# Performance work log

Measured on AMD Instinct MI355X. Metric: run time of the kernel, lower is better.

## Reference

```python
import jax, jax.numpy as jnp
import numpy as np

B, T, D = 32, 2048, 512
BATCH_SIZE = 32  # config.batch_size: number of MVN draws


def setup_inputs() -> dict:
    key = jax.random.key(0)
    k1, k2 = jax.random.split(key)
    x = jax.random.normal(k1, (B, T, D), dtype=jnp.float32)
    z = jax.random.normal(k2, (BATCH_SIZE, D), dtype=jnp.float32)  # standard-normal noise for reparameterized MVN draw
    return {"x": x, "z": z}


def reference(x, z):
    # mean over batch and time -> [D]
    mean = jnp.mean(x, axis=(0, 1))
    # per-batch covariance over time axis, then mean over batch -> [D, D]
    t = x.shape[1]
    xc = x - jnp.mean(x, axis=1, keepdims=True)
    # sum over b and t fused: equals mean_b( xc_b^T xc_b / (t-1) )
    cov = jnp.einsum('btd,bte->de', xc, xc) / ((t - 1) * x.shape[0])
    # multivariate normal draw via Cholesky reparameterization:
    # sample = mean + z @ L^T, L L^T = cov
    L = jnp.linalg.cholesky(cov)
    return mean + z @ L.T
```

## Files before the change

### kernel.cpp

```cpp
#include <hip/hip_runtime.h>

#define Dn 512
#define Bn 32
#define Tn 2048
#define BT 65536
#define NCHUNK 64
#define CHUNK_K 1024

typedef unsigned short u16;
typedef __attribute__((ext_vector_type(8))) short short8;
typedef __attribute__((ext_vector_type(4))) float floatx4;

__device__ __forceinline__ u16 f2bf(float f) {
    unsigned u = __float_as_uint(f);
    unsigned r = (u + 0x7FFFu + ((u >> 16) & 1u)) >> 16;
    return (u16)r;
}
__device__ __forceinline__ float bf2f(u16 s) { return __uint_as_float(((unsigned)s) << 16); }

#define GLL(gp, sp) __builtin_amdgcn_global_load_lds( \
    (const __attribute__((address_space(1))) void*)(gp), \
    (__attribute__((address_space(3))) void*)(sp), 16, 0, 0)

#define RLF(x, L) __uint_as_float(__builtin_amdgcn_readlane(__float_as_uint(x), (L)))

#define REP64(X) X(0) X(1) X(2) X(3) X(4) X(5) X(6) X(7) X(8) X(9) X(10) X(11) X(12) X(13) X(14) X(15) \
    X(16) X(17) X(18) X(19) X(20) X(21) X(22) X(23) X(24) X(25) X(26) X(27) X(28) X(29) X(30) X(31) \
    X(32) X(33) X(34) X(35) X(36) X(37) X(38) X(39) X(40) X(41) X(42) X(43) X(44) X(45) X(46) X(47) \
    X(48) X(49) X(50) X(51) X(52) X(53) X(54) X(55) X(56) X(57) X(58) X(59) X(60) X(61) X(62) X(63)
#define REPJH1(OP, K) OP(K,0) OP(K,1) OP(K,2) OP(K,3) OP(K,4) OP(K,5) OP(K,6) OP(K,7) OP(K,8) OP(K,9) \
    OP(K,10) OP(K,11) OP(K,12) OP(K,13) OP(K,14) OP(K,15) OP(K,16) OP(K,17) OP(K,18) OP(K,19) \
    OP(K,20) OP(K,21) OP(K,22) OP(K,23) OP(K,24) OP(K,25) OP(K,26) OP(K,27) OP(K,28) OP(K,29) \
    OP(K,30) OP(K,31)
#define REPJH2(OP, K) OP(K,32) OP(K,33) OP(K,34) OP(K,35) OP(K,36) OP(K,37) OP(K,38) OP(K,39) \
    OP(K,40) OP(K,41) OP(K,42) OP(K,43) OP(K,44) OP(K,45) OP(K,46) OP(K,47) OP(K,48) OP(K,49) \
    OP(K,50) OP(K,51) OP(K,52) OP(K,53) OP(K,54) OP(K,55) OP(K,56) OP(K,57) OP(K,58) OP(K,59) \
    OP(K,60) OP(K,61) OP(K,62) OP(K,63)
#define REPQA(OP, C) OP(C,0,0,0) OP(C,1,0,1) OP(C,2,0,2) OP(C,3,0,3) OP(C,4,1,0) OP(C,5,1,1) OP(C,6,1,2) OP(C,7,1,3) \
    OP(C,8,2,0) OP(C,9,2,1) OP(C,10,2,2) OP(C,11,2,3) OP(C,12,3,0) OP(C,13,3,1) OP(C,14,3,2) OP(C,15,3,3)
#define REPQB(OP, C) OP(C,16,4,0) OP(C,17,4,1) OP(C,18,4,2) OP(C,19,4,3) OP(C,20,5,0) OP(C,21,5,1) OP(C,22,5,2) OP(C,23,5,3) \
    OP(C,24,6,0) OP(C,25,6,1) OP(C,26,6,2) OP(C,27,6,3) OP(C,28,7,0) OP(C,29,7,1) OP(C,30,7,2) OP(C,31,7,3)
#define REPQC(OP, C) OP(C,32,8,0) OP(C,33,8,1) OP(C,34,8,2) OP(C,35,8,3) OP(C,36,9,0) OP(C,37,9,1) OP(C,38,9,2) OP(C,39,9,3) \
    OP(C,40,10,0) OP(C,41,10,1) OP(C,42,10,2) OP(C,43,10,3) OP(C,44,11,0) OP(C,45,11,1) OP(C,46,11,2) OP(C,47,11,3)
#define REPQD(OP, C) OP(C,48,12,0) OP(C,49,12,1) OP(C,50,12,2) OP(C,51,12,3) OP(C,52,13,0) OP(C,53,13,1) OP(C,54,13,2) OP(C,55,13,3) \
    OP(C,56,14,0) OP(C,57,14,1) OP(C,58,14,2) OP(C,59,14,3) OP(C,60,15,0) OP(C,61,15,1) OP(C,62,15,2) OP(C,63,15,3)
#define REPQ(OP, C) REPQA(OP, C) REPQB(OP, C) REPQC(OP, C) REPQD(OP, C)
#define REPW(OP) OP(0,0,1,2,3) OP(1,4,5,6,7) OP(2,8,9,10,11) OP(3,12,13,14,15) OP(4,16,17,18,19) \
    OP(5,20,21,22,23) OP(6,24,25,26,27) OP(7,28,29,30,31) OP(8,32,33,34,35) OP(9,36,37,38,39) \
    OP(10,40,41,42,43) OP(11,44,45,46,47) OP(12,48,49,50,51) OP(13,52,53,54,55) OP(14,56,57,58,59) \
    OP(15,60,61,62,63)

__global__ __launch_bounds__(256) void k_zero(float* __restrict__ mu) {
    floatx4 z = {0.f, 0.f, 0.f, 0.f};
    ((floatx4*)mu)[blockIdx.x * 256 + threadIdx.x] = z;
}

__global__ __launch_bounds__(256) void k_transpose(const float* __restrict__ x,
                                                   u16* __restrict__ Xt,
                                                   float* __restrict__ mu) {
    int tt = blockIdx.x;
    int dt = blockIdx.y;
    int b  = blockIdx.z;
    __shared__ u16 sT[64][68];
    int tid = threadIdx.x;
    int row = tid >> 4;
    int c4  = (tid & 15) * 4;
    const float* src = x + ((long)b * Tn + (long)tt * 64) * Dn + dt * 64;
#pragma unroll
    for (int q = 0; q < 4; q++) {
        int r = row + q * 16;
        floatx4 v = *(const floatx4*)(src + (long)r * Dn + c4);
        sT[c4 + 0][r] = f2bf(v[0]);
        sT[c4 + 1][r] = f2bf(v[1]);
        sT[c4 + 2][r] = f2bf(v[2]);
        sT[c4 + 3][r] = f2bf(v[3]);
    }
    __syncthreads();
    int drow = tid >> 3;
    int koff = (tid & 7) * 8;
    long kout = (long)b * Tn + (long)tt * 64 + koff;
#pragma unroll
    for (int p = 0; p < 2; p++) {
        int dr = drow + p * 32;
        u16 tmp[8];
        float s = 0.f;
#pragma unroll
        for (int j = 0; j < 8; j++) {
            tmp[j] = sT[dr][koff + j];
            s += bf2f(tmp[j]);
        }
        *(short8*)(Xt + (long)(dt * 64 + dr) * BT + kout) = *(short8*)tmp;
        s += __shfl_down(s, 4, 64);
        s += __shfl_down(s, 2, 64);
        s += __shfl_down(s, 1, 64);
        if ((tid & 7) == 0) atomicAdd(mu + b * 512 + dt * 64 + dr, s);
    }
}

__global__ __launch_bounds__(256, 3) void k_gram(const u16* __restrict__ Xt,
                                                 float* __restrict__ partial) {
    int chunk = blockIdx.x;
    int pos = blockIdx.y;
    int di = (pos < 4) ? 0 : (pos < 7) ? 1 : (pos < 9) ? 2 : 3;
    int start = di * 4 - (di * (di - 1)) / 2;
    int ei = di + (pos - start);
    int d0 = di * 128, e0 = ei * 128;

    __shared__ u16 sA[128 * 32];
    __shared__ u16 sB[128 * 32];
    int tid = threadIdx.x;
    int w = tid >> 6, l = tid & 63;
    int wm = w & 1, wn = w >> 1;
    long kbase = (long)chunk * CHUNK_K;
    int srow = w * 16 + (l >> 2);
    int sk = (l & 3) * 8;
    const u16* gA0 = Xt + (long)(d0 + srow) * BT + kbase + sk;
    const u16* gA1 = gA0 + 64l * BT;
    const u16* gB0 = Xt + (long)(e0 + srow) * BT + kbase + sk;
    const u16* gB1 = gB0 + 64l * BT;
    u16* sA0 = sA + (w * 16) * 32;
    u16* sA1 = sA0 + 64 * 32;
    u16* sB0 = sB + (w * 16) * 32;
    u16* sB1 = sB0 + 64 * 32;
    int m = l & 15, g = l >> 4;
    const u16* fA = sA + (wm * 64 + m) * 32 + g * 8;
    const u16* fB = sB + (wn * 64 + m) * 32 + g * 8;

    floatx4 acc[4][4] = {};
    for (int kk = 0; kk < CHUNK_K; kk += 32) {
        GLL(gA0 + kk, sA0);
        GLL(gA1 + kk, sA1);
        GLL(gB0 + kk, sB0);
        GLL(gB1 + kk, sB1);
        __syncthreads();
        short8 af[4], bfv[4];
#pragma unroll
        for (int i = 0; i < 4; i++) af[i] = *(const short8*)(fA + i * 16 * 32);
#pragma unroll
        for (int j = 0; j < 4; j++) bfv[j] = *(const short8*)(fB + j * 16 * 32);
#pragma unroll
        for (int i = 0; i < 4; i++)
#pragma unroll
            for (int j = 0; j < 4; j++)
                acc[i][j] = __builtin_amdgcn_mfma_f32_16x16x32_bf16(af[i], bfv[j], acc[i][j], 0, 0, 0);
        __syncthreads();
    }
    float* P = partial + (long)chunk * (512l * 512);
    int col = l & 15, rowg = (l >> 4) * 4;
#pragma unroll
    for (int i = 0; i < 4; i++)
#pragma unroll
        for (int j = 0; j < 4; j++) {
            int rr = d0 + wm * 64 + i * 16 + rowg;
            int cc = e0 + wn * 64 + j * 16 + col;
#pragma unroll
            for (int r = 0; r < 4; r++) P[(long)(rr + r) * 512 + cc] = acc[i][j][r];
        }
}

__global__ __launch_bounds__(256) void k_assemble(const float* __restrict__ partial,
                                                  const float* __restrict__ mu,
                                                  float* __restrict__ A) {
    int d = blockIdx.y;
    int e = blockIdx.x * 256 + threadIdx.x;
    int bd = d >> 7, be = e >> 7;
    long idx = (bd <= be) ? ((long)d * 512 + e) : ((long)e * 512 + d);
    float s = 0.f;
#pragma unroll
    for (int c = 0; c < NCHUNK; c++) s += partial[c * (512l * 512) + idx];
    float msum = 0.f;
#pragma unroll
    for (int b = 0; b < 32; b++) msum += mu[b * 512 + d] * mu[b * 512 + e];
    A[(long)d * 512 + e] = (s - msum * (1.0f / Tn)) * (1.0f / ((Tn - 1.0f) * Bn));
}

__global__ __launch_bounds__(256, 1) void k_chol_step(float* __restrict__ A,
                                                      float* __restrict__ L,
                                                      int kb) {
    const int k0 = kb * 64;
    const int tid = threadIdx.x;
    const int lane = tid & 63;
    const int wave = tid >> 6;
    int idx = blockIdx.x, ti = 0;
    while (idx > ti) { idx -= ti + 1; ti++; }
    const int tj = idx;
    const int row0 = k0 + 64 + ti * 64;
    const int col0 = k0 + 64 + tj * 64;
    __shared__ float sI[64 * 65];
    __shared__ float sJ[64 * 65];

    if (wave < 2) {
        const float* Dr = A + (long)(k0 + lane) * 512 + k0;
#define LDV(Q,A0,A1,A2,A3) floatx4 v##Q = *(const floatx4*)(Dr + 4*(Q));
        REPW(LDV)
#undef LDV
#define DECR(C,M,Mq,e) float r##M = v##Mq[(e)];
        REPQ(DECR, 0)
#undef DECR
        float vinv = 0.f;
#define SH1(K,J) float t##J = ((J) > (K)) ? RLF(lik, J) : 0.0f;
#define FM1(K,J) if ((J) > (K)) r##J = fmaf(nlik, t##J, r##J);
#define STEP(K) { float akk = RLF(r##K, K); float sd = sqrtf(akk); \
                  float inv = 1.0f / sd; float lik = (lane == (K)) ? sd : r##K * inv; \
                  r##K = lik; if (lane == (K)) vinv = inv; float nlik = -lik; \
                  { REPJH1(SH1, K) REPJH1(FM1, K) } { REPJH2(SH1, K) REPJH2(FM1, K) } }
        REP64(STEP)
#undef STEP
#undef FM1
#undef SH1
        if (blockIdx.x == 0 && wave == 0) {
            float* W = L + (long)(k0 + lane) * 512 + k0;
#define STW(Q,A0,A1,A2,A3) { floatx4 w; w[0]=r##A0; w[1]=r##A1; w[2]=r##A2; w[3]=r##A3; \
                             *(floatx4*)(W + 4*(Q)) = w; }
            REPW(STW)
#undef STW
        }

        const int sbase = (wave == 0) ? row0 : col0;
        const float* R = A + (long)(sbase + lane) * 512 + k0;
#define LDA(Q,A0,A1,A2,A3) floatx4 u##Q = *(const floatx4*)(R + 4*(Q));
        REPW(LDA)
#undef LDA
#define DECA(C,M,Mq,e) float a##M = u##Mq[(e)];
        REPQ(DECA, 0)
#undef DECA
#define TRL(C,M,Mq,e) float t##M = ((M) < (C)) ? RLF(r##M, C) : 0.0f;
#define TFM(C,M,Mq,e) if ((M) < (C)) acc##e = fmaf(a##M, t##M, acc##e);
#define TSTEP(C) { float acc0 = 0.f, acc1 = 0.f, acc2 = 0.f, acc3 = 0.f; \
                   { REPQA(TRL, C) REPQA(TFM, C) } { REPQB(TRL, C) REPQB(TFM, C) } \
                   { REPQC(TRL, C) REPQC(TFM, C) } { REPQD(TRL, C) REPQD(TFM, C) } \
                   float invC = RLF(vinv, C); \
                   a##C = (a##C - ((acc0 + acc1) + (acc2 + acc3))) * invC; }
        REP64(TSTEP)
#undef TSTEP
#undef TFM
#undef TRL
        float* sS = (wave == 0) ? sI : sJ;
#define STS(Q,A0,A1,A2,A3) { floatx4 w; w[0]=a##A0; w[1]=a##A1; w[2]=a##A2; w[3]=a##A3; \
                             *(floatx4*)(sS + lane * 65 + 4*(Q)) = w; }
        REPW(STS)
#undef STS
        if (ti == tj && wave == 0) {
            float* Wr = L + (long)(row0 + lane) * 512 + k0;
#define STA(Q,A0,A1,A2,A3) { floatx4 w; w[0]=a##A0; w[1]=a##A1; w[2]=a##A2; w[3]=a##A3; \
                             *(floatx4*)(Wr + 4*(Q)) = w; }
            REPW(STA)
#undef STA
        }
    }
    __syncthreads();

    {
        int ri = (tid >> 4) * 4, cj = (tid & 15) * 4;
        float acc[4][4] = {};
        for (int k = 0; k < 64; k += 4) {
            floatx4 av[4], bv[4];
#pragma unroll
            for (int ii = 0; ii < 4; ii++) av[ii] = *(const floatx4*)&sI[(ri + ii) * 65 + k];
#pragma unroll
            for (int jj = 0; jj < 4; jj++) bv[jj] = *(const floatx4*)&sJ[(cj + jj) * 65 + k];
#pragma unroll
            for (int ii = 0; ii < 4; ii++)
#pragma unroll
                for (int jj = 0; jj < 4; jj++)
#pragma unroll
                    for (int q = 0; q < 4; q++)
                        acc[ii][jj] = fmaf(av[ii][q], bv[jj][q], acc[ii][jj]);
        }
#pragma unroll
        for (int ii = 0; ii < 4; ii++) {
            float* dst = A + (long)(row0 + ri + ii) * 512 + col0 + cj;
            floatx4 old = *(const floatx4*)dst;
#pragma unroll
            for (int jj = 0; jj < 4; jj++) old[jj] -= acc[ii][jj];
            *(floatx4*)dst = old;
        }
    }
}

__global__ __launch_bounds__(64, 1) void k_chol_last(const float* __restrict__ A,
                                                     float* __restrict__ L) {
    const int k0 = 7 * 64;
    const int lane = threadIdx.x;
    const float* Dr = A + (long)(k0 + lane) * 512 + k0;
#define LDV(Q,A0,A1,A2,A3) floatx4 v##Q = *(const floatx4*)(Dr + 4*(Q));
    REPW(LDV)
#undef LDV
#define DECR(C,M,Mq,e) float r##M = v##Mq[(e)];
    REPQ(DECR, 0)
#undef DECR
#define SH1(K,J) float t##J = ((J) > (K)) ? RLF(lik, J) : 0.0f;
#define FM1(K,J) if ((J) > (K)) r##J = fmaf(nlik, t##J, r##J);
#define STEP(K) { float akk = RLF(r##K, K); float sd = sqrtf(akk); \
                  float inv = 1.0f / sd; float lik = (lane == (K)) ? sd : r##K * inv; \
                  r##K = lik; float nlik = -lik; \
                  { REPJH1(SH1, K) REPJH1(FM1, K) } { REPJH2(SH1, K) REPJH2(FM1, K) } }
    REP64(STEP)
#undef STEP
#undef FM1
#undef SH1
    float* W = L + (long)(k0 + lane) * 512 + k0;
#define STW(Q,A0,A1,A2,A3) { floatx4 w; w[0]=r##A0; w[1]=r##A1; w[2]=r##A2; w[3]=r##A3; \
                             *(floatx4*)(W + 4*(Q)) = w; }
    REPW(STW)
#undef STW
}

__global__ __launch_bounds__(512) void k_output(const float* __restrict__ z,
                                                const float* __restrict__ L,
                                                const float* __restrict__ mu,
                                                float* __restrict__ out) {
    int i = blockIdx.x, d = threadIdx.x;
    __shared__ float sz[512];
    sz[d] = z[(long)i * 512 + d];
    __syncthreads();
    float mean = 0.f;
#pragma unroll
    for (int b = 0; b < 32; b++) mean += mu[b * 512 + d];
    mean *= (1.0f / (32.0f * 2048.0f));
    const float* Lr = L + (long)d * 512;
    float acc = 0.f;
    int dmax = d + 1;
    int e4 = dmax & ~3;
    for (int e = 0; e < e4; e += 4) {
        floatx4 l = *(const floatx4*)(Lr + e);
        acc += l[0] * sz[e] + l[1] * sz[e + 1] + l[2] * sz[e + 2] + l[3] * sz[e + 3];
    }
    for (int e = e4; e < dmax; e++) acc += Lr[e] * sz[e];
    out[(long)i * 512 + d] = mean + acc;
}

extern "C" void kernel_launch(void* const* d_in, const int* in_sizes, int n_in,
                              void* d_out, int out_size, void* d_ws, size_t ws_size,
                              hipStream_t stream) {
    const float* x = (const float*)d_in[0];
    const float* z = (const float*)d_in[1];
    float* out = (float*)d_out;
    char* ws = (char*)d_ws;
    u16* Xt = (u16*)ws;
    float* mu = (float*)(ws + 67108864);
    float* partial = (float*)(ws + 67108864 + 65536);
    float* A = (float*)(ws + 67108864 + 65536 + 67108864);
    float* Lmat = (float*)(ws + 67108864 + 65536 + 67108864 + 1048576);

    k_zero<<<16, 256, 0, stream>>>(mu);
    k_transpose<<<dim3(32, 8, 32), 256, 0, stream>>>(x, Xt, mu);
    k_gram<<<dim3(NCHUNK, 10), 256, 0, stream>>>(Xt, partial);
    k_assemble<<<dim3(2, 512), 256, 0, stream>>>(partial, mu, A);
    for (int kb = 0; kb < 7; kb++) {
        int nb = 7 - kb;
        k_chol_step<<<nb * (nb + 1) / 2, 256, 0, stream>>>(A, Lmat, kb);
    }
    k_chol_last<<<1, 64, 0, stream>>>(A, Lmat);
    k_output<<<32, 512, 0, stream>>>(z, Lmat, mu, out);
}
```

Baseline: 558.5 us.

## Use precomputed inverse diagonal factor to replace serial triangular solves in Cholesky steps

Each Cholesky step no longer makes every block redo the 64x64 diagonal factorization and a serial readlane-based triangular solve. The next diagonal block is factored once, at the end of the previous step by block 0, along with the explicit inverse of its L factor, which is stored in a workspace buffer. Every block then computes its panel as a plain 64x64 matrix multiply against that inverse in shared memory. This removes the serial per-block dependency chain and the separate last kernel. The cost is more shared memory, a serial tail on block 0 in each step, and an explicit inverse that may lose some accuracy.

```diff
diff --git a/kernel.cpp b/kernel.cpp
--- a/kernel.cpp
+++ b/kernel.cpp
@@ -50,6 +50,22 @@
     OP(10,40,41,42,43) OP(11,44,45,46,47) OP(12,48,49,50,51) OP(13,52,53,54,55) OP(14,56,57,58,59) \
     OP(15,60,61,62,63)
 
+#define SH1(K,J) float t##J = ((J) > (K)) ? RLF(lik, J) : 0.0f;
+#define FM1(K,J) if ((J) > (K)) r##J = fmaf(nlik, t##J, r##J);
+#define FSTEP(K) { float akk = RLF(r##K, K); float sd = sqrtf(akk); \
+    float inv = 1.0f / sd; float lik = (lane == (K)) ? sd : r##K * inv; \
+    r##K = lik; if (lane == (K)) vinv = inv; float nlik = -lik; \
+    { REPJH1(SH1, K) REPJH1(FM1, K) } { REPJH2(SH1, K) REPJH2(FM1, K) } }
+#define ITL(C,M,Mq,e) float t##M = ((M) < (C)) ? RLF(r##M, C) : 0.0f;
+#define IFM(C,M,Mq,e) if ((M) < (C)) acc##e = fmaf(w##M, t##M, acc##e);
+#define ISTEP(C) { float acc0 = 0.f, acc1 = 0.f, acc2 = 0.f, acc3 = 0.f; \
+    { REPQA(ITL, C) REPQA(IFM, C) } { REPQB(ITL, C) REPQB(IFM, C) } \
+    { REPQC(ITL, C) REPQC(IFM, C) } { REPQD(ITL, C) REPQD(IFM, C) } \
+    float invC = RLF(vinv, C); \
+    w##C = (((lane == (C)) ? 1.0f : 0.0f) - ((acc0 + acc1) + (acc2 + acc3))) * invC; }
+#define DECW(C,M,Mq,e) float w##M = 0.f;
+#define DECR(C,M,Mq,e) float r##M = v##Mq[(e)];
+
 __global__ __launch_bounds__(256) void k_zero(float* __restrict__ mu) {
     floatx4 z = {0.f, 0.f, 0.f, 0.f};
     ((floatx4*)mu)[blockIdx.x * 256 + threadIdx.x] = z;
@@ -174,8 +190,32 @@
     A[(long)d * 512 + e] = (s - msum * (1.0f / Tn)) * (1.0f / ((Tn - 1.0f) * Bn));
 }
 
+__global__ __launch_bounds__(64, 1) void k_chol_boot(const float* __restrict__ A,
+                                                     float* __restrict__ L,
+                                                     float* __restrict__ Wb) {
+    const int lane = threadIdx.x;
+    const float* Dr = A + (long)lane * 512;
+#define LDV(Q,A0,A1,A2,A3) floatx4 v##Q = *(const floatx4*)(Dr + 4*(Q));
+    REPW(LDV)
+#undef LDV
+    REPQ(DECR, 0)
+    float vinv = 0.f;
+    REP64(FSTEP)
+    float* Wd = L + (long)lane * 512;
+#define STW(Q,A0,A1,A2,A3) { floatx4 o; o[0]=r##A0; o[1]=r##A1; o[2]=r##A2; o[3]=r##A3; \
+                             *(floatx4*)(Wd + 4*(Q)) = o; }
+    REPW(STW)
+#undef STW
+    REPQ(DECW, 0)
+    REP64(ISTEP)
+#define WSG(M) Wb[(M) * 64 + lane] = w##M;
+    REP64(WSG)
+#undef WSG
+}
+
 __global__ __launch_bounds__(256, 1) void k_chol_step(float* __restrict__ A,
                                                       float* __restrict__ L,
+                                                      float* __restrict__ Wb,
                                                       int kb) {
     const int k0 = kb * 64;
     const int tid = threadIdx.x;
@@ -186,124 +226,114 @@
     const int tj = idx;
     const int row0 = k0 + 64 + ti * 64;
     const int col0 = k0 + 64 + tj * 64;
-    __shared__ float sI[64 * 65];
-    __shared__ float sJ[64 * 65];
-
-    if (wave < 2) {
-        const float* Dr = A + (long)(k0 + lane) * 512 + k0;
+    __shared__ float sm[5 * 4160];
+    float* const sW = sm;
+    float* const sAi = sm + 4160;
+    float* const sAj = sm + 2 * 4160;
+    float* const sI = sm + 3 * 4160;
+    float* const sJ = sm + 4 * 4160;
+
+    {
+        int row = tid >> 4, c4 = (tid & 15) * 4;
+#pragma unroll
+        for (int q = 0; q < 4; q++) {
+            int rr = row + q * 16;
+            *(floatx4*)&sW[rr * 65 + c4] = *(const floatx4*)(Wb + rr * 64 + c4);
+            *(floatx4*)&sAi[rr * 65 + c4] = *(const floatx4*)(A + (long)(row0 + rr) * 512 + k0 + c4);
+            *(floatx4*)&sAj[rr * 65 + c4] = *(const floatx4*)(A + (long)(col0 + rr) * 512 + k0 + c4);
+        }
+    }
+    __syncthreads();
+
+    {
+        int ri = (tid >> 4) * 4, cj = (tid & 15) * 4;
+        float aci[4][4] = {}, acj[4][4] = {};
+        for (int mm = 0; mm < 64; mm += 4) {
+            floatx4 avi[4], avj[4], bw[4];
+#pragma unroll
+            for (int ii = 0; ii < 4; ii++) avi[ii] = *(const floatx4*)&sAi[(ri + ii) * 65 + mm];
+#pragma unroll
+            for (int ii = 0; ii < 4; ii++) avj[ii] = *(const floatx4*)&sAj[(ri + ii) * 65 + mm];
+#pragma unroll
+            for (int jj = 0; jj < 4; jj++) bw[jj] = *(const floatx4*)&sW[(cj + jj) * 65 + mm];
+#pragma unroll
+            for (int ii = 0; ii < 4; ii++)
+#pragma unroll
+                for (int jj = 0; jj < 4; jj++)
+#pragma unroll
+                    for (int q = 0; q < 4; q++) {
+                        aci[ii][jj] = fmaf(avi[ii][q], bw[jj][q], aci[ii][jj]);
+                        acj[ii][jj] = fmaf(avj[ii][q], bw[jj][q], acj[ii][jj]);
+                    }
+        }
+#pragma unroll
+        for (int ii = 0; ii < 4; ii++) {
+            floatx4 oi, oj;
+#pragma unroll
+            for (int jj = 0; jj < 4; jj++) { oi[jj] = aci[ii][jj]; oj[jj] = acj[ii][jj]; }
+            *(floatx4*)&sI[(ri + ii) * 65 + cj] = oi;
+            *(floatx4*)&sJ[(ri + ii) * 65 + cj] = oj;
+        }
+    }
+    __syncthreads();
+
+    if (ti == tj) {
+        int row = tid >> 4, c4 = (tid & 15) * 4;
+#pragma unroll
+        for (int q = 0; q < 4; q++) {
+            int rr = row + q * 16;
+            *(floatx4*)(L + (long)(row0 + rr) * 512 + k0 + c4) = *(const floatx4*)&sI[rr * 65 + c4];
+        }
+    }
+
+    {
+        int ri = (tid >> 4) * 4, cj = (tid & 15) * 4;
+        float acu[4][4] = {};
+        for (int mm = 0; mm < 64; mm += 4) {
+            floatx4 av[4], bv[4];
+#pragma unroll
+            for (int ii = 0; ii < 4; ii++) av[ii] = *(const floatx4*)&sI[(ri + ii) * 65 + mm];
+#pragma unroll
+            for (int jj = 0; jj < 4; jj++) bv[jj] = *(const floatx4*)&sJ[(cj + jj) * 65 + mm];
+#pragma unroll
+            for (int ii = 0; ii < 4; ii++)
+#pragma unroll
+                for (int jj = 0; jj < 4; jj++)
+#pragma unroll
+                    for (int q = 0; q < 4; q++)
+                        acu[ii][jj] = fmaf(av[ii][q], bv[jj][q], acu[ii][jj]);
+        }
+#pragma unroll
+        for (int ii = 0; ii < 4; ii++) {
+            float* dst = A + (long)(row0 + ri + ii) * 512 + col0 + cj;
+            floatx4 old = *(const floatx4*)dst;
+#pragma unroll
+            for (int jj = 0; jj < 4; jj++) old[jj] -= acu[ii][jj];
+            *(floatx4*)dst = old;
+            if (blockIdx.x == 0) *(floatx4*)&sAi[(ri + ii) * 65 + cj] = old;
+        }
+    }
+    __syncthreads();
+
+    if (blockIdx.x == 0 && wave == 0) {
+        const float* Dr = &sAi[lane * 65];
 #define LDV(Q,A0,A1,A2,A3) floatx4 v##Q = *(const floatx4*)(Dr + 4*(Q));
         REPW(LDV)
 #undef LDV
-#define DECR(C,M,Mq,e) float r##M = v##Mq[(e)];
         REPQ(DECR, 0)
-#undef DECR
         float vinv = 0.f;
-#define SH1(K,J) float t##J = ((J) > (K)) ? RLF(lik, J) : 0.0f;
-#define FM1(K,J) if ((J) > (K)) r##J = fmaf(nlik, t##J, r##J);
-#define STEP(K) { float akk = RLF(r##K, K); float sd = sqrtf(akk); \
-                  float inv = 1.0f / sd; float lik = (lane == (K)) ? sd : r##K * inv; \
-                  r##K = lik; if (lane == (K)) vinv = inv; float nlik = -lik; \
-                  { REPJH1(SH1, K) REPJH1(FM1, K) } { REPJH2(SH1, K) REPJH2(FM1, K) } }
-        REP64(STEP)
-#undef STEP
-#undef FM1
-#undef SH1
-        if (blockIdx.x == 0 && wave == 0) {
-            float* W = L + (long)(k0 + lane) * 512 + k0;
-#define STW(Q,A0,A1,A2,A3) { floatx4 w; w[0]=r##A0; w[1]=r##A1; w[2]=r##A2; w[3]=r##A3; \
-                             *(floatx4*)(W + 4*(Q)) = w; }
-            REPW(STW)
+        REP64(FSTEP)
+        float* Wd = L + (long)(k0 + 64 + lane) * 512 + k0 + 64;
+#define STW(Q,A0,A1,A2,A3) { floatx4 o; o[0]=r##A0; o[1]=r##A1; o[2]=r##A2; o[3]=r##A3; \
+                             *(floatx4*)(Wd + 4*(Q)) = o; }
+        REPW(STW)
 #undef STW
-        }
-
-        const int sbase = (wave == 0) ? row0 : col0;
-        const float* R = A + (long)(sbase + lane) * 512 + k0;
-#define LDA(Q,A0,A1,A2,A3) floatx4 u##Q = *(const floatx4*)(R + 4*(Q));
-        REPW(LDA)
-#undef LDA
-#define DECA(C,M,Mq,e) float a##M = u##Mq[(e)];
-        REPQ(DECA, 0)
-#undef DECA
-#define TRL(C,M,Mq,e) float t##M = ((M) < (C)) ? RLF(r##M, C) : 0.0f;
-#define TFM(C,M,Mq,e) if ((M) < (C)) acc##e = fmaf(a##M, t##M, acc##e);
-#define TSTEP(C) { float acc0 = 0.f, acc1 = 0.f, acc2 = 0.f, acc3 = 0.f; \
-                   { REPQA(TRL, C) REPQA(TFM, C) } { REPQB(TRL, C) REPQB(TFM, C) } \
-                   { REPQC(TRL, C) REPQC(TFM, C) } { REPQD(TRL, C) REPQD(TFM, C) } \
-                   float invC = RLF(vinv, C); \
-                   a##C = (a##C - ((acc0 + acc1) + (acc2 + acc3))) * invC; }
-        REP64(TSTEP)
-#undef TSTEP
-#undef TFM
-#undef TRL
-        float* sS = (wave == 0) ? sI : sJ;
-#define STS(Q,A0,A1,A2,A3) { floatx4 w; w[0]=a##A0; w[1]=a##A1; w[2]=a##A2; w[3]=a##A3; \
-                             *(floatx4*)(sS + lane * 65 + 4*(Q)) = w; }
-        REPW(STS)
-#undef STS
-        if (ti == tj && wave == 0) {
-            float* Wr = L + (long)(row0 + lane) * 512 + k0;
-#define STA(Q,A0,A1,A2,A3) { floatx4 w; w[0]=a##A0; w[1]=a##A1; w[2]=a##A2; w[3]=a##A3; \
-                             *(floatx4*)(Wr + 4*(Q)) = w; }
-            REPW(STA)
-#undef STA
-        }
-    }
-    __syncthreads();
-
-    {
-        int ri = (tid >> 4) * 4, cj = (tid & 15) * 4;
-        float acc[4][4] = {};
-        for (int k = 0; k < 64; k += 4) {
-            floatx4 av[4], bv[4];
-#pragma unroll
-            for (int ii = 0; ii < 4; ii++) av[ii] = *(const floatx4*)&sI[(ri + ii) * 65 + k];
-#pragma unroll
-            for (int jj = 0; jj < 4; jj++) bv[jj] = *(const floatx4*)&sJ[(cj + jj) * 65 + k];
-#pragma unroll
-            for (int ii = 0; ii < 4; ii++)
-#pragma unroll
-                for (int jj = 0; jj < 4; jj++)
-#pragma unroll
-                    for (int q = 0; q < 4; q++)
-                        acc[ii][jj] = fmaf(av[ii][q], bv[jj][q], acc[ii][jj]);
-        }
-#pragma unroll
-        for (int ii = 0; ii < 4; ii++) {
-            float* dst = A + (long)(row0 + ri + ii) * 512 + col0 + cj;
-            floatx4 old = *(const floatx4*)dst;
-#pragma unroll
-            for (int jj = 0; jj < 4; jj++) old[jj] -= acc[ii][jj];
-            *(floatx4*)dst = old;
-        }
-    }
-}
-
-__global__ __launch_bounds__(64, 1) void k_chol_last(const float* __restrict__ A,
-                                                     float* __restrict__ L) {
-    const int k0 = 7 * 64;
-    const int lane = threadIdx.x;
-    const float* Dr = A + (long)(k0 + lane) * 512 + k0;
-#define LDV(Q,A0,A1,A2,A3) floatx4 v##Q = *(const floatx4*)(Dr + 4*(Q));
-    REPW(LDV)
-#undef LDV
-#define DECR(C,M,Mq,e) float r##M = v##Mq[(e)];
-    REPQ(DECR, 0)
-#undef DECR
-#define SH1(K,J) float t##J = ((J) > (K)) ? RLF(lik, J) : 0.0f;
-#define FM1(K,J) if ((J) > (K)) r##J = fmaf(nlik, t##J, r##J);
-#define STEP(K) { float akk = RLF(r##K, K); float sd = sqrtf(akk); \
-                  float inv = 1.0f / sd; float lik = (lane == (K)) ? sd : r##K * inv; \
-                  r##K = lik; float nlik = -lik; \
-                  { REPJH1(SH1, K) REPJH1(FM1, K) } { REPJH2(SH1, K) REPJH2(FM1, K) } }
-    REP64(STEP)
-#undef STEP
-#undef FM1
-#undef SH1
-    float* W = L + (long)(k0 + lane) * 512 + k0;
-#define STW(Q,A0,A1,A2,A3) { floatx4 w; w[0]=r##A0; w[1]=r##A1; w[2]=r##A2; w[3]=r##A3; \
-                             *(floatx4*)(W + 4*(Q)) = w; }
-    REPW(STW)
-#undef STW
+        REPQ(DECW, 0)
+        REP64(ISTEP)
+#define WSG(M) Wb[(M) * 64 + lane] = w##M;
+        REP64(WSG)
+#undef WSG
+    }
 }
 
 __global__ __launch_bounds__(512) void k_output(const float* __restrict__ z,
@@ -323,8 +353,8 @@
     int dmax = d + 1;
     int e4 = dmax & ~3;
     for (int e = 0; e < e4; e += 4) {
-        floatx4 l = *(const floatx4*)(Lr + e);
-        acc += l[0] * sz[e] + l[1] * sz[e + 1] + l[2] * sz[e + 2] + l[3] * sz[e + 3];
+        floatx4 lv = *(const floatx4*)(Lr + e);
+        acc += lv[0] * sz[e] + lv[1] * sz[e + 1] + lv[2] * sz[e + 2] + lv[3] * sz[e + 3];
     }
     for (int e = e4; e < dmax; e++) acc += Lr[e] * sz[e];
     out[(long)i * 512 + d] = mean + acc;
@@ -342,15 +372,16 @@
     float* partial = (float*)(ws + 67108864 + 65536);
     float* A = (float*)(ws + 67108864 + 65536 + 67108864);
     float* Lmat = (float*)(ws + 67108864 + 65536 + 67108864 + 1048576);
+    float* Wbuf = (float*)(ws + 67108864 + 65536 + 67108864 + 1048576 + 1048576);
 
     k_zero<<<16, 256, 0, stream>>>(mu);
     k_transpose<<<dim3(32, 8, 32), 256, 0, stream>>>(x, Xt, mu);
     k_gram<<<dim3(NCHUNK, 10), 256, 0, stream>>>(Xt, partial);
     k_assemble<<<dim3(2, 512), 256, 0, stream>>>(partial, mu, A);
+    k_chol_boot<<<1, 64, 0, stream>>>(A, Lmat, Wbuf);
     for (int kb = 0; kb < 7; kb++) {
         int nb = 7 - kb;
-        k_chol_step<<<nb * (nb + 1) / 2, 256, 0, stream>>>(A, Lmat, kb);
-    }
-    k_chol_last<<<1, 64, 0, stream>>>(A, Lmat);
+        k_chol_step<<<nb * (nb + 1) / 2, 256, 0, stream>>>(A, Lmat, Wbuf, kb);
+    }
     k_output<<<32, 512, 0, stream>>>(z, Lmat, mu, out);
 }
```

Measured after the change: 935.0 us. 1.67x slower.
